# Optimization experiments

Measured on AMD Instinct MI355X. Metric: run time of the kernel, lower is better.

## Reference

```python
import jax, jax.numpy as jnp
import numpy as np

S_DIM, I_DIM, O_DIM = 1024, 2048, 1024
TOTAL = S_DIM + I_DIM + O_DIM  # 4096
INPUT_DIM, NUM_CLASSES, BATCH = 2048, 1000, 256


def setup_inputs() -> dict:
    key = jax.random.key(0)
    ks = jax.random.split(key, 6)
    x = jax.random.normal(ks[0], (BATCH, INPUT_DIM), dtype=jnp.float32)
    W = jax.random.normal(ks[1], (TOTAL, TOTAL), dtype=jnp.float32) * 0.02
    # torch Linear: weight [out, in], bias [out]
    in_w = jax.random.normal(ks[2], (S_DIM, INPUT_DIM), dtype=jnp.float32) * (1.0 / np.sqrt(INPUT_DIM))
    in_b = jax.random.normal(ks[3], (S_DIM,), dtype=jnp.float32) * 0.01
    out_w = jax.random.normal(ks[4], (NUM_CLASSES, O_DIM), dtype=jnp.float32) * (1.0 / np.sqrt(O_DIM))
    out_b = jax.random.normal(ks[5], (NUM_CLASSES,), dtype=jnp.float32) * 0.01
    return {"x": x, "W": W, "in_w": in_w, "in_b": in_b, "out_w": out_w, "out_b": out_b, "time_steps": 10}


def reference(x, W, in_w, in_b, out_w, out_b, time_steps):
    B = x.shape[0]
    S, I, O = S_DIM, I_DIM, O_DIM
    # slice effective W into 9 sub-blocks (use_lora=False -> W_eff = W)
    W_ss, W_sr, W_so = W[:S, :S], W[:S, S:S + I], W[:S, S + I:]
    W_rs, W_rr, W_ro = W[S:S + I, :S], W[S:S + I, S:S + I], W[S:S + I, S + I:]
    W_os, W_or, W_oo = W[S + I:, :S], W[S + I:, S:S + I], W[S + I:, S + I:]

    E = x @ in_w.T + in_b  # [B, S]
    gate = (jnp.arange(time_steps) % 5 == 0).astype(x.dtype)  # E injected when t%5==0

    init = (jnp.zeros((B, S), x.dtype), jnp.zeros((B, I), x.dtype), jnp.zeros((B, O), x.dtype))

    def step(carry, g):
        Ss, Is, Os = carry
        S_next = jax.nn.relu(Ss @ W_ss + g * E + Is @ W_rs + Os @ W_os)
        I_next = jax.nn.relu(Is @ W_rr + Ss @ W_sr + Os @ W_or)
        O_next = jax.nn.relu(Os @ W_oo + Is @ W_ro + Ss @ W_so)
        return (S_next, I_next, O_next), None

    (Ss, Is, Os), _ = jax.lax.scan(step, init, gate)
    return Os @ out_w.T + out_b  # [B, num_classes]
```

## Files before the change

### kernel.cpp

```cpp
#include <hip/hip_runtime.h>


typedef __bf16 bf16x8 __attribute__((ext_vector_type(8)));
typedef float  f32x16 __attribute__((ext_vector_type(16)));

#define TOTAL 4096
#define BATCH 256
#define INDIM 2048
#define SDIM  1024
#define NCLS  1000

#define MFMA(a, b, c) __builtin_amdgcn_mfma_f32_32x32x16_bf16((a), (b), (c), 0, 0, 0)

__device__ inline f32x16 zero16() {
    f32x16 v;
#pragma unroll
    for (int i = 0; i < 16; ++i) v[i] = 0.f;
    return v;
}

__device__ inline void swz_slot(const float* __restrict__ in, __bf16* __restrict__ out,
                                int C, int Rvalid, int t) {
    const int lane = t & 63;
    const int frag = t >> 6;
    const int kcN = C >> 4;
    const int rt = frag / kcN;
    const int kc = frag - rt * kcN;
    const int r = rt * 32 + (lane & 31);
    const int c = kc * 16 + (lane >> 5) * 8;
    alignas(16) __bf16 v[8];
    if (r < Rvalid) {
        const float* p = in + (size_t)r * C + c;
#pragma unroll
        for (int j = 0; j < 8; ++j) v[j] = (__bf16)p[j];
    } else {
#pragma unroll
        for (int j = 0; j < 8; ++j) v[j] = (__bf16)0.f;
    }
    *(ulonglong2*)(out + (size_t)t * 8) = *(const ulonglong2*)v;
}

__global__ __launch_bounds__(256) void k_prep(const float* __restrict__ W,
                                              const float* __restrict__ x,
                                              const float* __restrict__ in_w,
                                              const float* __restrict__ in_b,
                                              const float* __restrict__ out_w,
                                              __bf16* __restrict__ WT,
                                              __bf16* __restrict__ OWT,
                                              float* __restrict__ Ebuf,
                                              __bf16* __restrict__ H0) {
    __shared__ float t[64][65];
    const int bid = blockIdx.x;
    const int tid = threadIdx.x;
    if (bid < 256) {
        float* red = &t[0][0];
        const int mt = bid >> 5, nt = bid & 31;
        const int wave = tid >> 6, lane = tid & 63;
        const int l31 = lane & 31, kh = (lane >> 5) * 8;
        const int k0 = wave * 512;
        const float* Ax = x    + (size_t)(mt * 32 + l31) * INDIM + k0 + kh;
        const float* Bw = in_w + (size_t)(nt * 32 + l31) * INDIM + k0 + kh;
        f32x16 acc = zero16();
#pragma unroll 4
        for (int i = 0; i < 32; ++i) {
            const float* pa = Ax + i * 16;
            const float* pb = Bw + i * 16;
            float4 a0 = *(const float4*)pa, a1 = *(const float4*)(pa + 4);
            float4 b0 = *(const float4*)pb, b1 = *(const float4*)(pb + 4);
            bf16x8 a, b;
            a[0] = (__bf16)a0.x; a[1] = (__bf16)a0.y; a[2] = (__bf16)a0.z; a[3] = (__bf16)a0.w;
            a[4] = (__bf16)a1.x; a[5] = (__bf16)a1.y; a[6] = (__bf16)a1.z; a[7] = (__bf16)a1.w;
            b[0] = (__bf16)b0.x; b[1] = (__bf16)b0.y; b[2] = (__bf16)b0.z; b[3] = (__bf16)b0.w;
            b[4] = (__bf16)b1.x; b[5] = (__bf16)b1.y; b[6] = (__bf16)b1.z; b[7] = (__bf16)b1.w;
            acc = MFMA(a, b, acc);
        }
#pragma unroll
        for (int r = 0; r < 16; ++r) {
            int row = (r & 3) + 8 * (r >> 2) + 4 * (lane >> 5);
            red[wave * 1024 + row * 32 + l31] = acc[r];
        }
        __syncthreads();
        const int e0 = tid * 4;
        float4 s = {0.f, 0.f, 0.f, 0.f};
#pragma unroll
        for (int w = 0; w < 4; ++w) {
            float4 v = *(const float4*)&red[w * 1024 + e0];
            s.x += v.x; s.y += v.y; s.z += v.z; s.w += v.w;
        }
        const int row = e0 >> 5, col = e0 & 31;
        const int m = mt * 32 + row, n = nt * 32 + col;
        float v[4] = {s.x + in_b[n], s.y + in_b[n + 1], s.z + in_b[n + 2], s.w + in_b[n + 3]};
        *(float4*)(Ebuf + m * SDIM + n) = *(const float4*)v;
        alignas(8) __bf16 o[4];
#pragma unroll
        for (int j = 0; j < 4; ++j) o[j] = (__bf16)fmaxf(v[j], 0.f);
        const size_t frag = (size_t)(m >> 5) * (TOTAL / 16) + (n >> 4);
        const int lh = (m & 31) + 32 * ((n >> 3) & 1);
        *(ushort4*)(H0 + frag * 512 + lh * 8 + (n & 7)) = *(const ushort4*)o;
    } else if (bid < 4352) {
        const int wb = bid - 256;
        const int n0 = (wb & 63) * 64;
        const int k0 = (wb >> 6) * 64;
        const int rr = tid >> 4;
        const int cc = (tid & 15) * 4;
#pragma unroll
        for (int p = 0; p < 4; ++p) {
            const int k = p * 16 + rr;
            float4 v = *(const float4*)(W + (size_t)(k0 + k) * TOTAL + n0 + cc);
            t[cc][k] = v.x; t[cc + 1][k] = v.y; t[cc + 2][k] = v.z; t[cc + 3][k] = v.w;
        }
        __syncthreads();
#pragma unroll
        for (int s = tid; s < 512; s += 256) {
            const int frag = s >> 6;
            const int lane = s & 63;
            const int lrt = frag >> 2;
            const int lkc = frag & 3;
            const int nl = lrt * 32 + (lane & 31);
            const int kl = lkc * 16 + (lane >> 5) * 8;
            float4 f0 = *(const float4*)&t[nl][kl];
            float4 f1 = *(const float4*)&t[nl][kl + 4];
            bf16x8 v;
            v[0] = (__bf16)f0.x; v[1] = (__bf16)f0.y; v[2] = (__bf16)f0.z; v[3] = (__bf16)f0.w;
            v[4] = (__bf16)f1.x; v[5] = (__bf16)f1.y; v[6] = (__bf16)f1.z; v[7] = (__bf16)f1.w;
            const size_t fragG = (size_t)((n0 >> 5) + lrt) * (TOTAL / 16) + ((k0 >> 4) + lkc);
            *(bf16x8*)(WT + fragG * 512 + lane * 8) = v;
        }
    } else {
        swz_slot(out_w, OWT, 1024, NCLS, (bid - 4352) * 256 + tid);
    }
}

template <int CHUNKS>
__global__ __launch_bounds__(512, 2) void k_step(const __bf16* __restrict__ h,
                                                 const __bf16* __restrict__ WT,
                                                 const float* __restrict__ E,
                                                 const int gate,
                                                 __bf16* __restrict__ hn) {
    __shared__ float buf[4][4096];
    const int wave = threadIdx.x >> 6;
    const int lane = threadIdx.x & 63;
    const int xcd = blockIdx.x & 7;
    const int idx = blockIdx.x >> 3;
    const int mt = idx & 3;
    const int nt = xcd * 8 + (idx >> 2);
    constexpr int PER = CHUNKS >> 3;
    const int kc0 = wave * PER;

    const bf16x8* A0 = (const bf16x8*)h  + ((size_t)(mt * 2) * (TOTAL / 16) + kc0) * 64 + lane;
    const bf16x8* A1 = A0 + (size_t)(TOTAL / 16) * 64;
    const bf16x8* B0 = (const bf16x8*)WT + ((size_t)(nt * 2) * (TOTAL / 16) + kc0) * 64 + lane;
    const bf16x8* B1 = B0 + (size_t)(TOTAL / 16) * 64;

    f32x16 ac0 = zero16(), ac1 = zero16(), ac2 = zero16(), ac3 = zero16();
#pragma unroll 4
    for (int i = 0; i < PER; ++i) {
        const int off = i * 64;
        bf16x8 a0 = A0[off];
        bf16x8 a1 = A1[off];
        bf16x8 b0 = B0[off];
        bf16x8 b1 = B1[off];
        ac0 = MFMA(a0, b0, ac0);
        ac1 = MFMA(a0, b1, ac1);
        ac2 = MFMA(a1, b0, ac2);
        ac3 = MFMA(a1, b1, ac3);
    }

    f32x16 accs[4] = {ac0, ac1, ac2, ac3};
    if (wave >= 4) {
        float* b = buf[wave - 4];
#pragma unroll
        for (int c = 0; c < 4; ++c)
#pragma unroll
            for (int r = 0; r < 16; ++r)
                b[(c * 16 + r) * 64 + lane] = accs[c][r];
    }
    __syncthreads();
    if (wave < 4) {
        float* b = buf[wave];
#pragma unroll
        for (int c = 0; c < 4; ++c)
#pragma unroll
            for (int r = 0; r < 16; ++r) {
                const int i2 = (c * 16 + r) * 64 + lane;
                b[i2] += accs[c][r];
            }
    }
    __syncthreads();

    const int t = threadIdx.x;
    const int c = t >> 7;
    const int r = (t >> 3) & 15;
    const int l0 = (t & 7) * 8;
    const int base = (c * 16 + r) * 64 + l0;
    float4 s0 = {0.f, 0.f, 0.f, 0.f}, s1 = {0.f, 0.f, 0.f, 0.f};
#pragma unroll
    for (int w = 0; w < 4; ++w) {
        const float4* p = (const float4*)&buf[w][base];
        float4 v0 = p[0], v1 = p[1];
        s0.x += v0.x; s0.y += v0.y; s0.z += v0.z; s0.w += v0.w;
        s1.x += v1.x; s1.y += v1.y; s1.z += v1.z; s1.w += v1.w;
    }
    float v[8] = {s0.x, s0.y, s0.z, s0.w, s1.x, s1.y, s1.z, s1.w};
    const int ih = c >> 1, jh = c & 1;
    const int row = ih * 32 + (r & 3) + 8 * (r >> 2) + 4 * (l0 >> 5);
    const int col0 = jh * 32 + (l0 & 31);
    const int m = mt * 64 + row;
    const int n0g = nt * 64 + col0;
    if (gate && n0g < SDIM) {
        const float* Ep = E + m * SDIM + n0g;
#pragma unroll
        for (int j = 0; j < 8; ++j) v[j] += Ep[j];
    }
    alignas(16) __bf16 o[8];
#pragma unroll
    for (int j = 0; j < 8; ++j) o[j] = (__bf16)fmaxf(v[j], 0.f);
    const size_t frag = (size_t)(m >> 5) * (TOTAL / 16) + (n0g >> 4);
    const int lh = (m & 31) + 32 * ((n0g >> 3) & 1);
    *(ulonglong2*)(hn + frag * 512 + lh * 8) = *(const ulonglong2*)o;
}

__global__ __launch_bounds__(512, 4) void k_out(const __bf16* __restrict__ h,
                                                const __bf16* __restrict__ owt,
                                                const float* __restrict__ out_b,
                                                float* __restrict__ out) {
    __shared__ float red[8][1024];
    const int wave = threadIdx.x >> 6;
    const int lane = threadIdx.x & 63;
    const int mt = blockIdx.x >> 5;
    const int ct = blockIdx.x & 31;
    const int m0 = mt * 32, c0 = ct * 32;
    const int kcA0 = (3072 / 16) + wave * 8;
    const int kcB0 = wave * 8;
    const bf16x8* Ap = (const bf16x8*)h   + ((size_t)mt * (TOTAL / 16) + kcA0) * 64 + lane;
    const bf16x8* Bp = (const bf16x8*)owt + ((size_t)ct * (1024 / 16) + kcB0) * 64 + lane;
    f32x16 acc = zero16();
#pragma unroll
    for (int i = 0; i < 8; ++i)
        acc = MFMA(Ap[i * 64], Bp[i * 64], acc);
#pragma unroll
    for (int r = 0; r < 16; ++r) {
        int row = (r & 3) + 8 * (r >> 2) + 4 * (lane >> 5);
        red[wave][row * 32 + (lane & 31)] = acc[r];
    }
    __syncthreads();
    const int e0 = threadIdx.x * 2;
    float sx = 0.f, sy = 0.f;
#pragma unroll
    for (int w = 0; w < 8; ++w) {
        float2 v = *(const float2*)&red[w][e0];
        sx += v.x; sy += v.y;
    }
    const int row = e0 >> 5, col = e0 & 31;
    const int m = m0 + row;
    const int n = c0 + col;
    if (n < NCLS)     out[m * NCLS + n]     = sx + out_b[n];
    if (n + 1 < NCLS) out[m * NCLS + n + 1] = sy + out_b[n + 1];
}

extern "C" void kernel_launch(void* const* d_in, const int* in_sizes, int n_in,
                              void* d_out, int out_size, void* d_ws, size_t ws_size,
                              hipStream_t stream) {
    const float* x     = (const float*)d_in[0];
    const float* W     = (const float*)d_in[1];
    const float* in_w  = (const float*)d_in[2];
    const float* in_b  = (const float*)d_in[3];
    const float* out_w = (const float*)d_in[4];
    const float* out_b = (const float*)d_in[5];
    float* out = (float*)d_out;

    char* ws = (char*)d_ws;
    __bf16* WT  = (__bf16*)(ws + 0);
    __bf16* OWT = (__bf16*)(ws + 33554432);
    float*  Ebuf= (float*)(ws + 35651584);
    __bf16* H0  = (__bf16*)(ws + 36700160);
    __bf16* H1  = (__bf16*)(ws + 38797312);

    k_prep<<<4864, 256, 0, stream>>>(W, x, in_w, in_b, out_w, WT, OWT, Ebuf, H0);

    const __bf16* hs = H0;
    __bf16* hd = H1;
    for (int t = 1; t < 10; ++t) {
        const int gate = (t % 5 == 0) ? 1 : 0;
        if (t == 1)
            k_step<SDIM / 16><<<256, 512, 0, stream>>>(hs, WT, Ebuf, gate, hd);
        else
            k_step<TOTAL / 16><<<256, 512, 0, stream>>>(hs, WT, Ebuf, gate, hd);
        const __bf16* tmp = hs; hs = hd; hd = (__bf16*)tmp;
    }

    k_out<<<256, 512, 0, stream>>>(hs, OWT, out_b, out);
}
```

Baseline: 266.4 us.

## Double waves per step block with split-K and staged LDS reduction; widen W transpose tiles

The recurrent step kernel now runs 16 waves per block instead of 8. Each wave covers half as much of the K dimension, and the partial accumulators are summed through a multi-stage shared-memory reduction with extra barriers. This aims to add memory-level parallelism and latency hiding for the 256-block GEMV-like steps. In exchange it adds register pressure under the 1024-thread launch bound, more syncs, and narrower epilogue stores. Separately, the W transpose prep blocks now handle 128-column tiles, halving the block count.

```diff
diff --git a/kernel.cpp b/kernel.cpp
--- a/kernel.cpp
+++ b/kernel.cpp
@@ -49,7 +49,7 @@
                                               __bf16* __restrict__ OWT,
                                               float* __restrict__ Ebuf,
                                               __bf16* __restrict__ H0) {
-    __shared__ float t[64][65];
+    __shared__ float t[128][65];
     const int bid = blockIdx.x;
     const int tid = threadIdx.x;
     if (bid < 256) {
@@ -97,21 +97,24 @@
         const size_t frag = (size_t)(m >> 5) * (TOTAL / 16) + (n >> 4);
         const int lh = (m & 31) + 32 * ((n >> 3) & 1);
         *(ushort4*)(H0 + frag * 512 + lh * 8 + (n & 7)) = *(const ushort4*)o;
-    } else if (bid < 4352) {
+    } else if (bid < 2304) {
         const int wb = bid - 256;
-        const int n0 = (wb & 63) * 64;
-        const int k0 = (wb >> 6) * 64;
+        const int n0 = (wb & 31) * 128;
+        const int k0 = (wb >> 5) * 64;
         const int rr = tid >> 4;
-        const int cc = (tid & 15) * 4;
+        const int cc = (tid & 15) * 8;
 #pragma unroll
         for (int p = 0; p < 4; ++p) {
             const int k = p * 16 + rr;
-            float4 v = *(const float4*)(W + (size_t)(k0 + k) * TOTAL + n0 + cc);
-            t[cc][k] = v.x; t[cc + 1][k] = v.y; t[cc + 2][k] = v.z; t[cc + 3][k] = v.w;
+            const float* src = W + (size_t)(k0 + k) * TOTAL + n0 + cc;
+            float4 v0 = *(const float4*)src;
+            float4 v1 = *(const float4*)(src + 4);
+            t[cc][k] = v0.x; t[cc + 1][k] = v0.y; t[cc + 2][k] = v0.z; t[cc + 3][k] = v0.w;
+            t[cc + 4][k] = v1.x; t[cc + 5][k] = v1.y; t[cc + 6][k] = v1.z; t[cc + 7][k] = v1.w;
         }
         __syncthreads();
 #pragma unroll
-        for (int s = tid; s < 512; s += 256) {
+        for (int s = tid; s < 1024; s += 256) {
             const int frag = s >> 6;
             const int lane = s & 63;
             const int lrt = frag >> 2;
@@ -127,16 +130,16 @@
             *(bf16x8*)(WT + fragG * 512 + lane * 8) = v;
         }
     } else {
-        swz_slot(out_w, OWT, 1024, NCLS, (bid - 4352) * 256 + tid);
+        swz_slot(out_w, OWT, 1024, NCLS, (bid - 2304) * 256 + tid);
     }
 }
 
 template <int CHUNKS>
-__global__ __launch_bounds__(512, 2) void k_step(const __bf16* __restrict__ h,
-                                                 const __bf16* __restrict__ WT,
-                                                 const float* __restrict__ E,
-                                                 const int gate,
-                                                 __bf16* __restrict__ hn) {
+__global__ __launch_bounds__(1024, 4) void k_step(const __bf16* __restrict__ h,
+                                                  const __bf16* __restrict__ WT,
+                                                  const float* __restrict__ E,
+                                                  const int gate,
+                                                  __bf16* __restrict__ hn) {
     __shared__ float buf[4][4096];
     const int wave = threadIdx.x >> 6;
     const int lane = threadIdx.x & 63;
@@ -144,7 +147,7 @@
     const int idx = blockIdx.x >> 3;
     const int mt = idx & 3;
     const int nt = xcd * 8 + (idx >> 2);
-    constexpr int PER = CHUNKS >> 3;
+    constexpr int PER = CHUNKS >> 4;
     const int kc0 = wave * PER;
 
     const bf16x8* A0 = (const bf16x8*)h  + ((size_t)(mt * 2) * (TOTAL / 16) + kc0) * 64 + lane;
@@ -167,8 +170,29 @@
     }
 
     f32x16 accs[4] = {ac0, ac1, ac2, ac3};
-    if (wave >= 4) {
-        float* b = buf[wave - 4];
+#pragma unroll
+    for (int hi = 12; hi >= 4; hi -= 4) {
+        if (wave >= hi && wave < hi + 4) {
+            float* b = buf[wave - hi];
+#pragma unroll
+            for (int c = 0; c < 4; ++c)
+#pragma unroll
+                for (int r = 0; r < 16; ++r)
+                    b[(c * 16 + r) * 64 + lane] = accs[c][r];
+        }
+        __syncthreads();
+        if (wave >= hi - 4 && wave < hi) {
+            const float* b = buf[wave - (hi - 4)];
+#pragma unroll
+            for (int c = 0; c < 4; ++c)
+#pragma unroll
+                for (int r = 0; r < 16; ++r)
+                    accs[c][r] += b[(c * 16 + r) * 64 + lane];
+        }
+        __syncthreads();
+    }
+    if (wave < 4) {
+        float* b = buf[wave];
 #pragma unroll
         for (int c = 0; c < 4; ++c)
 #pragma unroll
@@ -176,32 +200,19 @@
                 b[(c * 16 + r) * 64 + lane] = accs[c][r];
     }
     __syncthreads();
-    if (wave < 4) {
-        float* b = buf[wave];
-#pragma unroll
-        for (int c = 0; c < 4; ++c)
-#pragma unroll
-            for (int r = 0; r < 16; ++r) {
-                const int i2 = (c * 16 + r) * 64 + lane;
-                b[i2] += accs[c][r];
-            }
-    }
-    __syncthreads();
 
     const int t = threadIdx.x;
-    const int c = t >> 7;
-    const int r = (t >> 3) & 15;
-    const int l0 = (t & 7) * 8;
+    const int c = t >> 8;
+    const int r = (t >> 4) & 15;
+    const int l0 = (t & 15) * 4;
     const int base = (c * 16 + r) * 64 + l0;
-    float4 s0 = {0.f, 0.f, 0.f, 0.f}, s1 = {0.f, 0.f, 0.f, 0.f};
+    float4 s = {0.f, 0.f, 0.f, 0.f};
 #pragma unroll
     for (int w = 0; w < 4; ++w) {
-        const float4* p = (const float4*)&buf[w][base];
-        float4 v0 = p[0], v1 = p[1];
-        s0.x += v0.x; s0.y += v0.y; s0.z += v0.z; s0.w += v0.w;
-        s1.x += v1.x; s1.y += v1.y; s1.z += v1.z; s1.w += v1.w;
-    }
-    float v[8] = {s0.x, s0.y, s0.z, s0.w, s1.x, s1.y, s1.z, s1.w};
+        float4 v = *(const float4*)&buf[w][base];
+        s.x += v.x; s.y += v.y; s.z += v.z; s.w += v.w;
+    }
+    float v[4] = {s.x, s.y, s.z, s.w};
     const int ih = c >> 1, jh = c & 1;
     const int row = ih * 32 + (r & 3) + 8 * (r >> 2) + 4 * (l0 >> 5);
     const int col0 = jh * 32 + (l0 & 31);
@@ -210,14 +221,14 @@
     if (gate && n0g < SDIM) {
         const float* Ep = E + m * SDIM + n0g;
 #pragma unroll
-        for (int j = 0; j < 8; ++j) v[j] += Ep[j];
-    }
-    alignas(16) __bf16 o[8];
-#pragma unroll
-    for (int j = 0; j < 8; ++j) o[j] = (__bf16)fmaxf(v[j], 0.f);
+        for (int j = 0; j < 4; ++j) v[j] += Ep[j];
+    }
+    alignas(8) __bf16 o[4];
+#pragma unroll
+    for (int j = 0; j < 4; ++j) o[j] = (__bf16)fmaxf(v[j], 0.f);
     const size_t frag = (size_t)(m >> 5) * (TOTAL / 16) + (n0g >> 4);
     const int lh = (m & 31) + 32 * ((n0g >> 3) & 1);
-    *(ulonglong2*)(hn + frag * 512 + lh * 8) = *(const ulonglong2*)o;
+    *(ushort4*)(hn + frag * 512 + lh * 8 + (n0g & 7)) = *(const ushort4*)o;
 }
 
 __global__ __launch_bounds__(512, 4) void k_out(const __bf16* __restrict__ h,
@@ -276,16 +287,16 @@
     __bf16* H0  = (__bf16*)(ws + 36700160);
     __bf16* H1  = (__bf16*)(ws + 38797312);
 
-    k_prep<<<4864, 256, 0, stream>>>(W, x, in_w, in_b, out_w, WT, OWT, Ebuf, H0);
+    k_prep<<<2816, 256, 0, stream>>>(W, x, in_w, in_b, out_w, WT, OWT, Ebuf, H0);
 
     const __bf16* hs = H0;
     __bf16* hd = H1;
     for (int t = 1; t < 10; ++t) {
         const int gate = (t % 5 == 0) ? 1 : 0;
         if (t == 1)
-            k_step<SDIM / 16><<<256, 512, 0, stream>>>(hs, WT, Ebuf, gate, hd);
+            k_step<SDIM / 16><<<256, 1024, 0, stream>>>(hs, WT, Ebuf, gate, hd);
         else
-            k_step<TOTAL / 16><<<256, 512, 0, stream>>>(hs, WT, Ebuf, gate, hd);
+            k_step<TOTAL / 16><<<256, 1024, 0, stream>>>(hs, WT, Ebuf, gate, hd);
         const __bf16* tmp = hs; hs = hd; hd = (__bf16*)tmp;
     }
 
```

Result: slower. 277.3 us (+4.1%).
